# Kernel optimization log

Measured on AMD Instinct MI355X. Metric: run time of the kernel, lower is better.

## Reference

```python
import jax, jax.numpy as jnp
import numpy as np

B, D, L = 32, 256, 1024        # batch, embedding_dim, compressed_len
K = 4096                       # num_embeddings (codebook size)
COMMITMENT_COST = 0.25


def setup_inputs() -> dict:
    key = jax.random.key(0)
    k1, k2 = jax.random.split(key)
    inputs = jax.random.normal(k1, (B, D, L), dtype=jnp.float32)
    embedding = jax.random.normal(k2, (K, D), dtype=jnp.float32)  # codebook
    return {"inputs": inputs, "embedding": embedding}


def reference(inputs, embedding):
    # [B, D, L] -> [B, L, D], flatten to [N, D]
    x = jnp.transpose(inputs, (0, 2, 1))
    flat = x.reshape(-1, D)  # [N, D], N = B*L

    # squared Euclidean distances to each code: [N, K]
    distances = (
        jnp.sum(flat * flat, axis=1, keepdims=True)
        + jnp.sum(embedding * embedding, axis=1)
        - 2.0 * jnp.matmul(flat, embedding.T)
    )
    encoding_indices = jnp.argmin(distances, axis=1)          # [N]
    encodings = jax.nn.one_hot(encoding_indices, K, dtype=jnp.float32)  # [N, K]

    # quantize via gather (same math as one_hot @ embedding)
    quantized = embedding[encoding_indices].reshape(x.shape)  # [B, L, D]

    # commitment loss (EMA module: only e_latent term, quantized detached)
    e_latent_loss = jnp.mean((jax.lax.stop_gradient(quantized) - x) ** 2)
    loss = COMMITMENT_COST * e_latent_loss

    # straight-through estimator
    quantized_st = x + jax.lax.stop_gradient(quantized - x)

    # perplexity from average code usage
    avg_probs = jnp.mean(encodings, axis=0)  # [K]
    perplexity = jnp.exp(-jnp.sum(avg_probs * jnp.log(avg_probs + 1e-10)))

    quantized_out = jnp.transpose(quantized_st, (0, 2, 1))  # [B, D, L]
    return (loss, quantized_out, perplexity, embedding,
            encoding_indices[:, None], encodings)
```

## Files before the change

kernel.cpp:

```cpp
#include <hip/hip_runtime.h>
#include <float.h>
#include <math.h>

typedef __attribute__((ext_vector_type(8))) short bf16x8;
typedef __attribute__((ext_vector_type(4))) float f32x4;

#define O_Q    1
#define O_PERP 8388609
#define O_EMB  8388610
#define O_IDX  9437186
#define O_ENC  9469954

#define W_CB   1048576
#define W_CNT  1052672
#define W_BS   1056768

#define MARGIN 0.01f

__device__ __forceinline__ unsigned short bf16_rne(float x) {
    unsigned u = __float_as_uint(x);
    unsigned r = u + 0x7FFFu + ((u >> 16) & 1u);
    return (unsigned short)(r >> 16);
}

__device__ __forceinline__ void gld_lds16(const void* g, void* l) {
    __builtin_amdgcn_global_load_lds(
        (const __attribute__((address_space(1))) unsigned int*)g,
        (__attribute__((address_space(3))) unsigned int*)l, 16, 0, 0);
}

__device__ __forceinline__ unsigned long long u64min(unsigned long long a, unsigned long long b){ return a < b ? a : b; }
__device__ __forceinline__ unsigned long long u64max(unsigned long long a, unsigned long long b){ return a > b ? a : b; }

__device__ __forceinline__ unsigned long long packkey(float s, int k) {
    unsigned u = __float_as_uint(s);
    u = (u & 0x80000000u) ? ~u : (u | 0x80000000u);
    return ((unsigned long long)u << 32) | (unsigned)k;
}
__device__ __forceinline__ float unpackf(unsigned long long key) {
    unsigned u = (unsigned)(key >> 32);
    u = (u & 0x80000000u) ? (u & 0x7FFFFFFFu) : ~u;
    return __uint_as_float(u);
}

__global__ __launch_bounds__(256)
void k_prepE(const float* __restrict__ E, char* __restrict__ ETpk)
{
    int gid = blockIdx.x * 256 + threadIdx.x;
    int code = gid >> 5, oct = gid & 31;
    const float* ep = E + (size_t)code * 256 + oct * 8;
    float4 a = *(const float4*)ep, c4 = *(const float4*)(ep + 4);
    float v[8] = {a.x, a.y, a.z, a.w, c4.x, c4.y, c4.z, c4.w};
    unsigned hw[8], lw[8];
#pragma unroll
    for (int i = 0; i < 8; ++i) {
        unsigned short h = bf16_rne(v[i]);
        float hf = __uint_as_float((unsigned)h << 16);
        hw[i] = h; lw[i] = bf16_rne(v[i] - hf);
    }
    uint4 vh = {hw[0]|(hw[1]<<16), hw[2]|(hw[3]<<16), hw[4]|(hw[5]<<16), hw[6]|(hw[7]<<16)};
    uint4 vl = {lw[0]|(lw[1]<<16), lw[2]|(lw[3]<<16), lw[4]|(lw[5]<<16), lw[6]|(lw[7]<<16)};
    int kt = code >> 8, cf = (code >> 4) & 15, row = code & 15;
    int dtv = oct >> 2, c = oct & 3;
    size_t chunk = (size_t)(kt * 8 + dtv) * 32768;
    *(uint4*)(ETpk + chunk + (size_t)((0*16 + cf) * 64 + (c*16 + row)) * 16) = vh;
    *(uint4*)(ETpk + chunk + (size_t)((1*16 + cf) * 64 + (c*16 + row)) * 16) = vl;
}

__global__ __launch_bounds__(256)
void k_cbias(const float* __restrict__ E, float* __restrict__ cb)
{
    const int tid = threadIdx.x;
    const int k   = blockIdx.x * 16 + (tid >> 4);
    const int ch  = tid & 15;
    const float* p = E + (size_t)k * 256 + ch * 16;
    float s = 0.f;
#pragma unroll
    for (int i = 0; i < 4; ++i) {
        float4 v = *(const float4*)(p + i * 4);
        s += v.x*v.x + v.y*v.y + v.z*v.z + v.w*v.w;
    }
#pragma unroll
    for (int m = 1; m < 16; m <<= 1) s += __shfl_xor(s, m, 64);
    if (ch == 0) cb[k] = 0.5f * s;
}

__global__ __launch_bounds__(512, 1)
void k_main(const float* __restrict__ X, const char* __restrict__ ETpk,
            const float* __restrict__ cbh, const float* __restrict__ E,
            float* __restrict__ out, int* __restrict__ counts,
            float* __restrict__ bscore)
{
    extern __shared__ char lds[];
    char* Alds = lds;
    char* Bsl  = lds + 65536;

    const int tid  = threadIdx.x;
    const int lane = tid & 63;
    const int wid  = tid >> 6;
    const int wm   = wid >> 2;
    const int wn   = wid & 3;
    const int n0   = blockIdx.x * 64;
    const int b    = n0 >> 10;
    const int l0   = n0 & 1023;
    const size_t xbase = (size_t)b * 262144 + l0;
    float* encB = out + (size_t)O_ENC + (size_t)n0 * 4096;

    f32x4 acc[2][4];
#pragma unroll
    for (int mi = 0; mi < 2; ++mi)
#pragma unroll
        for (int nj = 0; nj < 4; ++nj) acc[mi][nj] = (f32x4){0.f,0.f,0.f,0.f};

    float s1[8], s2[8];
    unsigned ipack[8];
#pragma unroll
    for (int s = 0; s < 8; ++s) { s1[s] = FLT_MAX; s2[s] = FLT_MAX; ipack[s] = 0; }

    auto stageB = [&](int rnd, int slot) {
        const char* src = ETpk + (size_t)rnd * 32768;
        char* dst = Bsl + slot * 32768;
#pragma unroll
        for (int i = 0; i < 4; ++i)
            gld_lds16(src + i*8192 + tid*16, dst + i*8192 + tid*16);
    };

    stageB(0, 0);
    stageB(1, 1);
    {
        const int t = tid & 63;
        const int g = tid >> 6;
#pragma unroll
        for (int jj = 0; jj < 4; ++jj) {
            const int j  = g + jj * 8;
            const int ks = j >> 2, c = j & 3;
            const float* xp = X + xbase + (size_t)(j * 8) * 1024 + t;
            float v[8];
#pragma unroll
            for (int i = 0; i < 8; ++i) v[i] = xp[(size_t)i * 1024];
            unsigned hw[8], lw[8];
#pragma unroll
            for (int i = 0; i < 8; ++i) {
                unsigned short h = bf16_rne(v[i]);
                float hf = __uint_as_float((unsigned)h << 16);
                hw[i] = h; lw[i] = bf16_rne(v[i] - hf);
            }
            uint4 vh = {hw[0]|(hw[1]<<16), hw[2]|(hw[3]<<16), hw[4]|(hw[5]<<16), hw[6]|(hw[7]<<16)};
            uint4 vl = {lw[0]|(lw[1]<<16), lw[2]|(lw[3]<<16), lw[4]|(lw[5]<<16), lw[6]|(lw[7]<<16)};
            char* d0 = Alds + ks * 8192 + (t >> 4) * 1024 + (c * 16 + (t & 15)) * 16;
            *(uint4*)d0          = vh;
            *(uint4*)(d0 + 4096) = vl;
        }
    }
    __syncthreads();

#pragma unroll 1
    for (int rd = 0; rd < 128; ++rd) {
        const char* A  = Alds + (rd & 7) * 8192;
        const char* Bp = Bsl + (rd % 3) * 32768;
        const int r2  = (rd + 2 < 128) ? rd + 2 : 127;
        stageB(r2, (rd + 2) % 3);
        {
            float2 z2 = make_float2(0.f, 0.f);
            float* zb = encB + (size_t)rd * 2048 + tid * 2;
            *(float2*)zb            = z2;
            *(float2*)(zb + 1024)   = z2;
        }

        {
            bf16x8 ah[2], al[2];
#pragma unroll
            for (int mi = 0; mi < 2; ++mi) {
                ah[mi] = *(const bf16x8*)(A + (wm*2 + mi)*1024 + lane*16);
                al[mi] = *(const bf16x8*)(A + 4096 + (wm*2 + mi)*1024 + lane*16);
            }
#pragma unroll
            for (int nj = 0; nj < 4; ++nj) {
                bf16x8 bh = *(const bf16x8*)(Bp + (wn*4 + nj)*1024 + lane*16);
                bf16x8 bl = *(const bf16x8*)(Bp + 16384 + (wn*4 + nj)*1024 + lane*16);
#pragma unroll
                for (int mi = 0; mi < 2; ++mi) {
                    acc[mi][nj] = __builtin_amdgcn_mfma_f32_16x16x32_bf16(ah[mi], bh, acc[mi][nj], 0, 0, 0);
                    acc[mi][nj] = __builtin_amdgcn_mfma_f32_16x16x32_bf16(al[mi], bh, acc[mi][nj], 0, 0, 0);
                    acc[mi][nj] = __builtin_amdgcn_mfma_f32_16x16x32_bf16(ah[mi], bl, acc[mi][nj], 0, 0, 0);
                }
            }
        }

        if ((rd & 7) == 7) {
            const int kt = rd >> 3;
            const int cb0 = kt * 256 + wn * 64 + (lane & 15);
            float cbv[4];
#pragma unroll
            for (int nj = 0; nj < 4; ++nj) cbv[nj] = cbh[cb0 + nj * 16];
#pragma unroll
            for (int mi = 0; mi < 2; ++mi)
#pragma unroll
                for (int q = 0; q < 4; ++q) {
                    const int slot = mi * 4 + q;
#pragma unroll
                    for (int nj = 0; nj < 4; ++nj) {
                        float s = cbv[nj] - acc[mi][nj][q];
                        unsigned code = (unsigned)(cb0 + nj * 16);
                        if (s < s1[slot]) {
                            s2[slot] = s1[slot];
                            ipack[slot] = ((ipack[slot] & 0xFFFFu) << 16) | code;
                            s1[slot] = s;
                        } else if (s < s2[slot]) {
                            s2[slot] = s;
                            ipack[slot] = (ipack[slot] & 0xFFFFu) | (code << 16);
                        }
                        acc[mi][nj][q] = 0.f;
                    }
                }
        }

        asm volatile("s_waitcnt vmcnt(6)" ::: "memory");
        __builtin_amdgcn_s_barrier();
    }

    __syncthreads();

    unsigned long long key1[8], key2[8];
#pragma unroll
    for (int s = 0; s < 8; ++s) {
        key1[s] = packkey(s1[s], (int)(ipack[s] & 0xFFFFu));
        key2[s] = packkey(s2[s], (int)(ipack[s] >> 16));
    }
#pragma unroll
    for (int m = 1; m < 16; m <<= 1) {
#pragma unroll
        for (int s = 0; s < 8; ++s) {
            unsigned long long o1 = __shfl_xor(key1[s], m, 64);
            unsigned long long o2 = __shfl_xor(key2[s], m, 64);
            unsigned long long lo = u64min(key1[s], o1);
            unsigned long long hi = u64min(u64max(key1[s], o1), u64min(key2[s], o2));
            key1[s] = lo; key2[s] = hi;
        }
    }

    unsigned long long* scr = (unsigned long long*)lds;
    int* ids  = (int*)(lds + 4096);
    float* wp = (float*)(lds + 4096 + 256);
    if ((lane & 15) == 0) {
#pragma unroll
        for (int mi = 0; mi < 2; ++mi)
#pragma unroll
            for (int q = 0; q < 4; ++q) {
                int slot = mi * 4 + q;
                int tl = wm * 32 + mi * 16 + ((lane >> 4) << 2) + q;
                scr[(tl * 4 + wn) * 2    ] = key1[slot];
                scr[(tl * 4 + wn) * 2 + 1] = key2[slot];
            }
    }
    __syncthreads();

    if (tid < 64) {
        unsigned long long a1 = scr[tid * 8], a2 = scr[tid * 8 + 1];
#pragma unroll
        for (int w = 1; w < 4; ++w) {
            unsigned long long b1 = scr[(tid * 4 + w) * 2];
            unsigned long long b2 = scr[(tid * 4 + w) * 2 + 1];
            unsigned long long lo = u64min(a1, b1);
            unsigned long long hi = u64min(u64max(a1, b1), u64min(a2, b2));
            a1 = lo; a2 = hi;
        }
        int k = (int)(a1 & 0xFFFFFFFFull);
        float g1 = unpackf(a1), g2 = unpackf(a2);
        if (g2 - g1 <= MARGIN) {
            int ka = k, kb = (int)(a2 & 0xFFFFFFFFull);
            float d1 = 0.f, d2 = 0.f;
            for (int d = 0; d < 256; d += 2) {
                float xv0 = X[xbase + (size_t)d * 1024 + tid];
                float xv1 = X[xbase + (size_t)(d + 1) * 1024 + tid];
                float e10 = E[(size_t)ka * 256 + d], e11 = E[(size_t)ka * 256 + d + 1];
                float e20 = E[(size_t)kb * 256 + d], e21 = E[(size_t)kb * 256 + d + 1];
                float f10 = xv0 - e10, f11 = xv1 - e11;
                float f20 = xv0 - e20, f21 = xv1 - e21;
                d1 += f10 * f10 + f11 * f11;
                d2 += f20 * f20 + f21 * f21;
            }
            if (d2 < d1 || (d2 == d1 && kb < ka)) k = kb;
        }
        ids[tid] = k;
        out[(size_t)O_IDX + n0 + tid] = (float)k;
        atomicAdd(&counts[k], 1);
        out[(size_t)O_ENC + (size_t)(n0 + tid) * 4096 + k] = 1.0f;
    }
    __syncthreads();

    float dl = 0.f;
#pragma unroll 4
    for (int r = 0; r < 32; ++r) {
        int lin = r * 512 + tid;
        int d = lin >> 6, t = lin & 63;
        float q  = E[(size_t)ids[t] * 256 + d];
        float xv = X[xbase + (size_t)d * 1024 + t];
        out[(size_t)O_Q + xbase + (size_t)d * 1024 + t] = xv + (q - xv);
        float df = q - xv;
        dl += df * df;
    }
#pragma unroll
    for (int m = 1; m < 64; m <<= 1) dl += __shfl_xor(dl, m, 64);
    if (lane == 0) wp[wid] = dl;
    __syncthreads();
    if (tid == 0) {
        float s = 0.f;
#pragma unroll
        for (int w = 0; w < 8; ++w) s += wp[w];
        bscore[blockIdx.x] = s;
    }
}

__global__ __launch_bounds__(256)
void k_final(const float* __restrict__ bscore, const int* __restrict__ counts,
             float* __restrict__ out)
{
    const int tid = threadIdx.x;
    float s = bscore[tid] + bscore[tid + 256];
    float h = 0.f;
#pragma unroll
    for (int i = 0; i < 16; ++i) {
        float p = (float)counts[tid * 16 + i] * (1.0f / 32768.f);
        h += p * logf(p + 1e-10f);
    }
#pragma unroll
    for (int m = 1; m < 64; m <<= 1) {
        s += __shfl_xor(s, m, 64);
        h += __shfl_xor(h, m, 64);
    }
    __shared__ float rs[4], rh[4];
    if ((tid & 63) == 0) { rs[tid >> 6] = s; rh[tid >> 6] = h; }
    __syncthreads();
    if (tid == 0) {
        float S = rs[0] + rs[1] + rs[2] + rs[3];
        float H = rh[0] + rh[1] + rh[2] + rh[3];
        out[0]      = 0.25f * S / 8388608.f;
        out[O_PERP] = expf(-H);
    }
}

extern "C" void kernel_launch(void* const* d_in, const int* in_sizes, int n_in,
                              void* d_out, int out_size, void* d_ws, size_t ws_size,
                              hipStream_t stream)
{
    (void)in_sizes; (void)n_in; (void)out_size; (void)ws_size;
    const float* X = (const float*)d_in[0];
    const float* E = (const float*)d_in[1];
    float* out = (float*)d_out;
    float* ws  = (float*)d_ws;
    char*  ETpk   = (char*)ws;
    float* cbh    = ws + W_CB;
    int*   counts = (int*)(ws + W_CNT);
    float* bsc    = ws + W_BS;

    hipMemsetAsync(counts, 0, 4096 * sizeof(int), stream);
    k_prepE<<<512, 256, 0, stream>>>(E, ETpk);
    k_cbias<<<256, 256, 0, stream>>>(E, cbh);
    hipFuncSetAttribute(reinterpret_cast<const void*>(&k_main),
                        hipFuncAttributeMaxDynamicSharedMemorySize, 163840);
    k_main <<<512, 512, 163840, stream>>>(X, ETpk, cbh, E, out, counts, bsc);
    k_final<<<1, 256, 0, stream>>>(bsc, counts, out);
    hipMemcpyAsync(out + O_EMB, E, (size_t)4096 * 256 * sizeof(float),
                   hipMemcpyDeviceToDevice, stream);
}
```

Measured before the change: 400.4 us.

## Drop codebook low-part MFMA, halve row tile, rescore wide-margin candidates exactly

The distance GEMM now multiplies the split-bf16 inputs only against the high bf16 part of the codebook. That removes one of three MFMAs per step and halves the codebook bytes staged into LDS. Each block now handles 32 rows instead of 64, which halves LDS use, doubles the grid and allows more blocks per CU. The argmin reduction changes from shuffle-merged top-2 keys to a per-row scan over 64 column candidates in LDS. Every candidate within a widened margin of 0.4 is then rescored exactly in fp32. The lower precision makes more rows need rescoring, and keeping only top-2 per column could miss a true minimum if several close codes fall in the same column.

```diff
diff --git a/kernel.cpp b/kernel.cpp
--- a/kernel.cpp
+++ b/kernel.cpp
@@ -15,7 +15,7 @@
 #define W_CNT  1052672
 #define W_BS   1056768
 
-#define MARGIN 0.01f
+#define MARGIN 0.4f
 
 __device__ __forceinline__ unsigned short bf16_rne(float x) {
     unsigned u = __float_as_uint(x);
@@ -30,7 +30,6 @@
 }
 
 __device__ __forceinline__ unsigned long long u64min(unsigned long long a, unsigned long long b){ return a < b ? a : b; }
-__device__ __forceinline__ unsigned long long u64max(unsigned long long a, unsigned long long b){ return a > b ? a : b; }
 
 __device__ __forceinline__ unsigned long long packkey(float s, int k) {
     unsigned u = __float_as_uint(s);
@@ -85,7 +84,7 @@
     if (ch == 0) cb[k] = 0.5f * s;
 }
 
-__global__ __launch_bounds__(512, 1)
+__global__ __launch_bounds__(512, 4)
 void k_main(const float* __restrict__ X, const char* __restrict__ ETpk,
             const float* __restrict__ cbh, const float* __restrict__ E,
             float* __restrict__ out, int* __restrict__ counts,
@@ -93,194 +92,172 @@
 {
     extern __shared__ char lds[];
     char* Alds = lds;
-    char* Bsl  = lds + 65536;
+    char* Bsl  = lds + 32768;
 
     const int tid  = threadIdx.x;
     const int lane = tid & 63;
     const int wid  = tid >> 6;
     const int wm   = wid >> 2;
     const int wn   = wid & 3;
-    const int n0   = blockIdx.x * 64;
+    const int n0   = blockIdx.x * 32;
     const int b    = n0 >> 10;
     const int l0   = n0 & 1023;
     const size_t xbase = (size_t)b * 262144 + l0;
     float* encB = out + (size_t)O_ENC + (size_t)n0 * 4096;
 
-    f32x4 acc[2][4];
-#pragma unroll
-    for (int mi = 0; mi < 2; ++mi)
-#pragma unroll
-        for (int nj = 0; nj < 4; ++nj) acc[mi][nj] = (f32x4){0.f,0.f,0.f,0.f};
-
-    float s1[8], s2[8];
-    unsigned ipack[8];
-#pragma unroll
-    for (int s = 0; s < 8; ++s) { s1[s] = FLT_MAX; s2[s] = FLT_MAX; ipack[s] = 0; }
+    f32x4 acc[4];
+#pragma unroll
+    for (int nj = 0; nj < 4; ++nj) acc[nj] = (f32x4){0.f,0.f,0.f,0.f};
+
+    float s1[4], s2v[4];
+    unsigned ipack[4];
+#pragma unroll
+    for (int s = 0; s < 4; ++s) { s1[s] = FLT_MAX; s2v[s] = FLT_MAX; ipack[s] = 0; }
 
     auto stageB = [&](int rnd, int slot) {
         const char* src = ETpk + (size_t)rnd * 32768;
-        char* dst = Bsl + slot * 32768;
-#pragma unroll
-        for (int i = 0; i < 4; ++i)
+        char* dst = Bsl + slot * 16384;
+#pragma unroll
+        for (int i = 0; i < 2; ++i)
             gld_lds16(src + i*8192 + tid*16, dst + i*8192 + tid*16);
     };
 
     stageB(0, 0);
     stageB(1, 1);
-    {
-        const int t = tid & 63;
-        const int g = tid >> 6;
-#pragma unroll
-        for (int jj = 0; jj < 4; ++jj) {
-            const int j  = g + jj * 8;
-            const int ks = j >> 2, c = j & 3;
-            const float* xp = X + xbase + (size_t)(j * 8) * 1024 + t;
-            float v[8];
-#pragma unroll
-            for (int i = 0; i < 8; ++i) v[i] = xp[(size_t)i * 1024];
-            unsigned hw[8], lw[8];
-#pragma unroll
-            for (int i = 0; i < 8; ++i) {
-                unsigned short h = bf16_rne(v[i]);
-                float hf = __uint_as_float((unsigned)h << 16);
-                hw[i] = h; lw[i] = bf16_rne(v[i] - hf);
+#pragma unroll
+    for (int pi = 0; pi < 2; ++pi) {
+        const int p = pi * 512 + tid;
+        const int t = p & 31, j = p >> 5;
+        const int ks = j >> 2, c = j & 3;
+        const float* xp = X + xbase + (size_t)(j * 8) * 1024 + t;
+        float v[8];
+#pragma unroll
+        for (int i = 0; i < 8; ++i) v[i] = xp[(size_t)i * 1024];
+        unsigned hw[8], lw[8];
+#pragma unroll
+        for (int i = 0; i < 8; ++i) {
+            unsigned short h = bf16_rne(v[i]);
+            float hf = __uint_as_float((unsigned)h << 16);
+            hw[i] = h; lw[i] = bf16_rne(v[i] - hf);
+        }
+        uint4 vh = {hw[0]|(hw[1]<<16), hw[2]|(hw[3]<<16), hw[4]|(hw[5]<<16), hw[6]|(hw[7]<<16)};
+        uint4 vl = {lw[0]|(lw[1]<<16), lw[2]|(lw[3]<<16), lw[4]|(lw[5]<<16), lw[6]|(lw[7]<<16)};
+        char* d0 = Alds + ks * 4096 + (t >> 4) * 1024 + (c * 16 + (t & 15)) * 16;
+        *(uint4*)d0          = vh;
+        *(uint4*)(d0 + 2048) = vl;
+    }
+    __syncthreads();
+
+#pragma unroll 1
+    for (int kt = 0; kt < 16; ++kt) {
+#pragma unroll 1
+        for (int ks = 0; ks < 8; ++ks) {
+            const int rd = kt * 8 + ks;
+            const char* A  = Alds + ks * 4096 + wm * 1024;
+            const char* Bp = Bsl + (rd % 3) * 16384;
+            const int r2 = (rd + 2 < 128) ? rd + 2 : 127;
+            stageB(r2, (rd + 2) % 3);
+            {
+                const int lin = rd * 1024 + tid * 2;
+                *(float2*)(encB + (size_t)(lin >> 12) * 4096 + (lin & 4095)) =
+                    make_float2(0.f, 0.f);
             }
-            uint4 vh = {hw[0]|(hw[1]<<16), hw[2]|(hw[3]<<16), hw[4]|(hw[5]<<16), hw[6]|(hw[7]<<16)};
-            uint4 vl = {lw[0]|(lw[1]<<16), lw[2]|(lw[3]<<16), lw[4]|(lw[5]<<16), lw[6]|(lw[7]<<16)};
-            char* d0 = Alds + ks * 8192 + (t >> 4) * 1024 + (c * 16 + (t & 15)) * 16;
-            *(uint4*)d0          = vh;
-            *(uint4*)(d0 + 4096) = vl;
-        }
-    }
-    __syncthreads();
-
-#pragma unroll 1
-    for (int rd = 0; rd < 128; ++rd) {
-        const char* A  = Alds + (rd & 7) * 8192;
-        const char* Bp = Bsl + (rd % 3) * 32768;
-        const int r2  = (rd + 2 < 128) ? rd + 2 : 127;
-        stageB(r2, (rd + 2) % 3);
-        {
-            float2 z2 = make_float2(0.f, 0.f);
-            float* zb = encB + (size_t)rd * 2048 + tid * 2;
-            *(float2*)zb            = z2;
-            *(float2*)(zb + 1024)   = z2;
-        }
-
-        {
-            bf16x8 ah[2], al[2];
-#pragma unroll
-            for (int mi = 0; mi < 2; ++mi) {
-                ah[mi] = *(const bf16x8*)(A + (wm*2 + mi)*1024 + lane*16);
-                al[mi] = *(const bf16x8*)(A + 4096 + (wm*2 + mi)*1024 + lane*16);
-            }
+            bf16x8 ah = *(const bf16x8*)(A + lane * 16);
+            bf16x8 al = *(const bf16x8*)(A + 2048 + lane * 16);
 #pragma unroll
             for (int nj = 0; nj < 4; ++nj) {
                 bf16x8 bh = *(const bf16x8*)(Bp + (wn*4 + nj)*1024 + lane*16);
-                bf16x8 bl = *(const bf16x8*)(Bp + 16384 + (wn*4 + nj)*1024 + lane*16);
-#pragma unroll
-                for (int mi = 0; mi < 2; ++mi) {
-                    acc[mi][nj] = __builtin_amdgcn_mfma_f32_16x16x32_bf16(ah[mi], bh, acc[mi][nj], 0, 0, 0);
-                    acc[mi][nj] = __builtin_amdgcn_mfma_f32_16x16x32_bf16(al[mi], bh, acc[mi][nj], 0, 0, 0);
-                    acc[mi][nj] = __builtin_amdgcn_mfma_f32_16x16x32_bf16(ah[mi], bl, acc[mi][nj], 0, 0, 0);
+                acc[nj] = __builtin_amdgcn_mfma_f32_16x16x32_bf16(ah, bh, acc[nj], 0, 0, 0);
+                acc[nj] = __builtin_amdgcn_mfma_f32_16x16x32_bf16(al, bh, acc[nj], 0, 0, 0);
+            }
+            asm volatile("s_waitcnt vmcnt(3)" ::: "memory");
+            __builtin_amdgcn_s_barrier();
+        }
+        {
+            const int cb0 = kt * 256 + wn * 64 + (lane & 15);
+            float cbv[4];
+#pragma unroll
+            for (int nj = 0; nj < 4; ++nj) cbv[nj] = cbh[cb0 + nj * 16];
+#pragma unroll
+            for (int q = 0; q < 4; ++q)
+#pragma unroll
+                for (int nj = 0; nj < 4; ++nj) {
+                    float s = cbv[nj] - acc[nj][q];
+                    unsigned code = (unsigned)(cb0 + nj * 16);
+                    if (s < s1[q]) {
+                        s2v[q] = s1[q];
+                        ipack[q] = ((ipack[q] & 0xFFFFu) << 16) | code;
+                        s1[q] = s;
+                    } else if (s < s2v[q]) {
+                        s2v[q] = s;
+                        ipack[q] = (ipack[q] & 0xFFFFu) | (code << 16);
+                    }
+                    acc[nj][q] = 0.f;
+                }
+        }
+    }
+
+    asm volatile("s_waitcnt vmcnt(0)" ::: "memory");
+    __syncthreads();
+
+    ulonglong2* scr = (ulonglong2*)lds;
+    int*   ids = (int*)(lds + 32768);
+    float* wp  = (float*)(lds + 32768 + 128);
+    {
+        const int col = wn * 16 + (lane & 15);
+#pragma unroll
+        for (int q = 0; q < 4; ++q) {
+            const int t = wm * 16 + ((lane >> 4) << 2) + q;
+            ulonglong2 kk;
+            kk.x = packkey(s1[q],  (int)(ipack[q] & 0xFFFFu));
+            kk.y = packkey(s2v[q], (int)(ipack[q] >> 16));
+            scr[t * 64 + col] = kk;
+        }
+    }
+    __syncthreads();
+
+    if (tid < 32) {
+        const ulonglong2* row = scr + tid * 64;
+        unsigned long long m = 0xFFFFFFFFFFFFFFFFull;
+#pragma unroll 1
+        for (int i0 = 0; i0 < 64; ++i0) {
+            int i = (2 * tid + i0) & 63;
+            m = u64min(m, row[i].x);
+        }
+        int k = (int)(m & 0xFFFFull);
+        const float thr = unpackf(m) + MARGIN;
+        int cnt = 0;
+#pragma unroll 1
+        for (int i0 = 0; i0 < 64; ++i0) {
+            int i = (2 * tid + i0) & 63;
+            ulonglong2 kk = row[i];
+            cnt += (unpackf(kk.x) <= thr) + (unpackf(kk.y) <= thr);
+        }
+        if (cnt > 1) {
+            float bd = FLT_MAX; int bi = 0x7FFFFFFF;
+#pragma unroll 1
+            for (int i0 = 0; i0 < 64; ++i0) {
+                int i = (2 * tid + i0) & 63;
+                ulonglong2 kk = row[i];
+#pragma unroll
+                for (int h = 0; h < 2; ++h) {
+                    unsigned long long key = h ? kk.y : kk.x;
+                    if (unpackf(key) <= thr) {
+                        int c = (int)(key & 0xFFFFull);
+                        float d = 0.f;
+                        for (int dd = 0; dd < 256; dd += 2) {
+                            float xv0 = X[xbase + (size_t)dd * 1024 + tid];
+                            float xv1 = X[xbase + (size_t)(dd + 1) * 1024 + tid];
+                            float e0 = E[(size_t)c * 256 + dd];
+                            float e1 = E[(size_t)c * 256 + dd + 1];
+                            float f0 = xv0 - e0, f1 = xv1 - e1;
+                            d += f0 * f0 + f1 * f1;
+                        }
+                        if (d < bd || (d == bd && c < bi)) { bd = d; bi = c; }
+                    }
                 }
             }
-        }
-
-        if ((rd & 7) == 7) {
-            const int kt = rd >> 3;
-            const int cb0 = kt * 256 + wn * 64 + (lane & 15);
-            float cbv[4];
-#pragma unroll
-            for (int nj = 0; nj < 4; ++nj) cbv[nj] = cbh[cb0 + nj * 16];
-#pragma unroll
-            for (int mi = 0; mi < 2; ++mi)
-#pragma unroll
-                for (int q = 0; q < 4; ++q) {
-                    const int slot = mi * 4 + q;
-#pragma unroll
-                    for (int nj = 0; nj < 4; ++nj) {
-                        float s = cbv[nj] - acc[mi][nj][q];
-                        unsigned code = (unsigned)(cb0 + nj * 16);
-                        if (s < s1[slot]) {
-                            s2[slot] = s1[slot];
-                            ipack[slot] = ((ipack[slot] & 0xFFFFu) << 16) | code;
-                            s1[slot] = s;
-                        } else if (s < s2[slot]) {
-                            s2[slot] = s;
-                            ipack[slot] = (ipack[slot] & 0xFFFFu) | (code << 16);
-                        }
-                        acc[mi][nj][q] = 0.f;
-                    }
-                }
-        }
-
-        asm volatile("s_waitcnt vmcnt(6)" ::: "memory");
-        __builtin_amdgcn_s_barrier();
-    }
-
-    __syncthreads();
-
-    unsigned long long key1[8], key2[8];
-#pragma unroll
-    for (int s = 0; s < 8; ++s) {
-        key1[s] = packkey(s1[s], (int)(ipack[s] & 0xFFFFu));
-        key2[s] = packkey(s2[s], (int)(ipack[s] >> 16));
-    }
-#pragma unroll
-    for (int m = 1; m < 16; m <<= 1) {
-#pragma unroll
-        for (int s = 0; s < 8; ++s) {
-            unsigned long long o1 = __shfl_xor(key1[s], m, 64);
-            unsigned long long o2 = __shfl_xor(key2[s], m, 64);
-            unsigned long long lo = u64min(key1[s], o1);
-            unsigned long long hi = u64min(u64max(key1[s], o1), u64min(key2[s], o2));
-            key1[s] = lo; key2[s] = hi;
-        }
-    }
-
-    unsigned long long* scr = (unsigned long long*)lds;
-    int* ids  = (int*)(lds + 4096);
-    float* wp = (float*)(lds + 4096 + 256);
-    if ((lane & 15) == 0) {
-#pragma unroll
-        for (int mi = 0; mi < 2; ++mi)
-#pragma unroll
-            for (int q = 0; q < 4; ++q) {
-                int slot = mi * 4 + q;
-                int tl = wm * 32 + mi * 16 + ((lane >> 4) << 2) + q;
-                scr[(tl * 4 + wn) * 2    ] = key1[slot];
-                scr[(tl * 4 + wn) * 2 + 1] = key2[slot];
-            }
-    }
-    __syncthreads();
-
-    if (tid < 64) {
-        unsigned long long a1 = scr[tid * 8], a2 = scr[tid * 8 + 1];
-#pragma unroll
-        for (int w = 1; w < 4; ++w) {
-            unsigned long long b1 = scr[(tid * 4 + w) * 2];
-            unsigned long long b2 = scr[(tid * 4 + w) * 2 + 1];
-            unsigned long long lo = u64min(a1, b1);
-            unsigned long long hi = u64min(u64max(a1, b1), u64min(a2, b2));
-            a1 = lo; a2 = hi;
-        }
-        int k = (int)(a1 & 0xFFFFFFFFull);
-        float g1 = unpackf(a1), g2 = unpackf(a2);
-        if (g2 - g1 <= MARGIN) {
-            int ka = k, kb = (int)(a2 & 0xFFFFFFFFull);
-            float d1 = 0.f, d2 = 0.f;
-            for (int d = 0; d < 256; d += 2) {
-                float xv0 = X[xbase + (size_t)d * 1024 + tid];
-                float xv1 = X[xbase + (size_t)(d + 1) * 1024 + tid];
-                float e10 = E[(size_t)ka * 256 + d], e11 = E[(size_t)ka * 256 + d + 1];
-                float e20 = E[(size_t)kb * 256 + d], e21 = E[(size_t)kb * 256 + d + 1];
-                float f10 = xv0 - e10, f11 = xv1 - e11;
-                float f20 = xv0 - e20, f21 = xv1 - e21;
-                d1 += f10 * f10 + f11 * f11;
-                d2 += f20 * f20 + f21 * f21;
-            }
-            if (d2 < d1 || (d2 == d1 && kb < ka)) k = kb;
+            k = bi;
         }
         ids[tid] = k;
         out[(size_t)O_IDX + n0 + tid] = (float)k;
@@ -291,9 +268,9 @@
 
     float dl = 0.f;
 #pragma unroll 4
-    for (int r = 0; r < 32; ++r) {
+    for (int r = 0; r < 16; ++r) {
         int lin = r * 512 + tid;
-        int d = lin >> 6, t = lin & 63;
+        int d = lin >> 5, t = lin & 31;
         float q  = E[(size_t)ids[t] * 256 + d];
         float xv = X[xbase + (size_t)d * 1024 + t];
         out[(size_t)O_Q + xbase + (size_t)d * 1024 + t] = xv + (q - xv);
@@ -317,7 +294,7 @@
              float* __restrict__ out)
 {
     const int tid = threadIdx.x;
-    float s = bscore[tid] + bscore[tid + 256];
+    float s = bscore[tid] + bscore[tid + 256] + bscore[tid + 512] + bscore[tid + 768];
     float h = 0.f;
 #pragma unroll
     for (int i = 0; i < 16; ++i) {
@@ -358,8 +335,8 @@
     k_prepE<<<512, 256, 0, stream>>>(E, ETpk);
     k_cbias<<<256, 256, 0, stream>>>(E, cbh);
     hipFuncSetAttribute(reinterpret_cast<const void*>(&k_main),
-                        hipFuncAttributeMaxDynamicSharedMemorySize, 163840);
-    k_main <<<512, 512, 163840, stream>>>(X, ETpk, cbh, E, out, counts, bsc);
+                        hipFuncAttributeMaxDynamicSharedMemorySize, 81920);
+    k_main <<<1024, 512, 81920, stream>>>(X, ETpk, cbh, E, out, counts, bsc);
     k_final<<<1, 256, 0, stream>>>(bsc, counts, out);
     hipMemcpyAsync(out + O_EMB, E, (size_t)4096 * 256 * sizeof(float),
                    hipMemcpyDeviceToDevice, stream);
```

Result: faster. 378.7 us (-5.4%).
